# Kernel tuning notes

Measured on AMD Instinct MI355X. Metric: run time of the kernel, lower is better.

## Reference

```python
import jax, jax.numpy as jnp
import numpy as np

B, N_ELEM, N_NODES, E2 = 4096, 2048, 1024, 4096


def setup_inputs() -> dict:
    key = jax.random.key(0)
    k = jax.random.split(key, 7)
    return {
        "EA": jax.random.normal(k[0], (B, N_ELEM), dtype=jnp.float32),
        "e": jax.random.normal(k[1], (B, N_ELEM), dtype=jnp.float32),
        "q": jax.random.normal(k[2], (B, N_NODES, 2), dtype=jnp.float32),
        "r": jax.random.normal(k[3], (B, N_NODES, 2), dtype=jnp.float32),
        "vecs": jax.random.normal(k[4], (E2, 2), dtype=jnp.float32),
        "node_ids": jax.random.randint(k[5], (E2,), 0, N_NODES, dtype=jnp.int32),
        "elem_ids": jax.random.randint(k[6], (E2,), 0, N_ELEM, dtype=jnp.int32),
    }


def reference(EA, e, q, r, vecs, node_ids, elem_ids):
    # axial_forces = EA * e : [B, N_ELEM]
    axial = EA * e
    # gather per incidence entry and scale by the 2-vector: [B, E2, 2]
    contrib = axial[:, elem_ids][..., None] * vecs[None, :, :]
    n_sample, n_nodes = q.shape[0], q.shape[1]
    # scatter-add contributions into per-node residual: [B, N_NODES, 2]
    residual = jnp.zeros((n_sample, n_nodes, 2), dtype=EA.dtype)
    residual = residual.at[:, node_ids, :].add(contrib)
    residual = residual - q - r
    return jnp.mean(jnp.square(residual))
```

## Files before the change

kernel.cpp:

```cpp
#include <hip/hip_runtime.h>

#define B_SAMPLES 4096
#define N_ELEM    2048
#define N_NODES   1024
#define E2        4096
#define BLOCK     512
#define SLOTS     32
#define S         4
#define NPT       (N_NODES / BLOCK)
#define MAIN_BLOCKS (B_SAMPLES / S)

#define WS_CNT_OFF   0
#define WS_ELL_OFF   4096

__global__ __launch_bounds__(256) void neq_zero_kernel(
    float4* __restrict__ ell, int* __restrict__ cnt)
{
    const int i = blockIdx.x * 256 + threadIdx.x;
    ell[i] = make_float4(0.f, 0.f, 0.f, 0.f);
    if (i < N_NODES) cnt[i] = 0;
}

__global__ __launch_bounds__(256) void neq_build_kernel(
    const float* __restrict__ vecs, const int* __restrict__ node_ids,
    const int* __restrict__ elem_ids, int* __restrict__ cnt,
    float4* __restrict__ ell)
{
    const int j = blockIdx.x * 256 + threadIdx.x;
    int nid = node_ids[j];
    int eid = elem_ids[j];
    float2 v = ((const float2*)vecs)[j];
    int slot = atomicAdd(&cnt[nid], 1);
    if (slot < SLOTS) {
        ell[slot * N_NODES + nid] = make_float4(v.x, v.y, __int_as_float(eid), 0.f);
    }
}

__global__ __launch_bounds__(BLOCK, 4) void neq_main_kernel(
    const float* __restrict__ EA, const float* __restrict__ e,
    const float* __restrict__ q,  const float* __restrict__ r,
    const int* __restrict__ cnt, const float4* __restrict__ ell,
    float* __restrict__ out)
{
    __shared__ float4 axial4[N_ELEM];
    __shared__ float red[BLOCK / 64];

    const int b0 = blockIdx.x * S;
    const int t = threadIdx.x;

#pragma unroll
    for (int i = 0; i < N_ELEM / BLOCK; ++i) {
        int eid = t + i * BLOCK;
        float4 p;
        const float* EAp = EA + (size_t)b0 * N_ELEM + eid;
        const float* ep  = e  + (size_t)b0 * N_ELEM + eid;
        p.x = EAp[0 * N_ELEM] * ep[0 * N_ELEM];
        p.y = EAp[1 * N_ELEM] * ep[1 * N_ELEM];
        p.z = EAp[2 * N_ELEM] * ep[2 * N_ELEM];
        p.w = EAp[3 * N_ELEM] * ep[3 * N_ELEM];
        axial4[eid] = p;
    }

    int c0 = min(cnt[t], SLOTS);
    int c1 = min(cnt[t + BLOCK], SLOTS);
    int kmax = max(c0, c1);
    __syncthreads();

    float accx[NPT][S] = {};
    float accy[NPT][S] = {};
    for (int k = 0; k < kmax; ++k) {
        const float4* row = ell + k * N_NODES + t;
#pragma unroll
        for (int i = 0; i < NPT; ++i) {
            int ci = (i == 0) ? c0 : c1;
            if (k < ci) {
                float4 pk = row[i * BLOCK];
                int eid = __float_as_int(pk.z);
                float4 ax = axial4[eid];
                accx[i][0] += ax.x * pk.x;  accy[i][0] += ax.x * pk.y;
                accx[i][1] += ax.y * pk.x;  accy[i][1] += ax.y * pk.y;
                accx[i][2] += ax.z * pk.x;  accy[i][2] += ax.z * pk.y;
                accx[i][3] += ax.w * pk.x;  accy[i][3] += ax.w * pk.y;
            }
        }
    }

    float acc = 0.f;
#pragma unroll
    for (int s = 0; s < S; ++s) {
        const float2* q2 = (const float2*)(q + (size_t)(b0 + s) * N_NODES * 2);
        const float2* r2 = (const float2*)(r + (size_t)(b0 + s) * N_NODES * 2);
#pragma unroll
        for (int i = 0; i < NPT; ++i) {
            int n = t + i * BLOCK;
            float2 qv = q2[n];
            float2 rv = r2[n];
            float x = accx[i][s] - qv.x - rv.x;
            float y = accy[i][s] - qv.y - rv.y;
            acc += x * x + y * y;
        }
    }

#pragma unroll
    for (int off = 32; off > 0; off >>= 1)
        acc += __shfl_down(acc, off, 64);
    if ((t & 63) == 0) red[t >> 6] = acc;
    __syncthreads();
    if (t == 0) {
        float s = 0.f;
#pragma unroll
        for (int w = 0; w < BLOCK / 64; ++w) s += red[w];
        const float inv_n = 1.0f / (float)((size_t)B_SAMPLES * N_NODES * 2);
        atomicAdd(out, s * inv_n);
    }
}

extern "C" void kernel_launch(void* const* d_in, const int* in_sizes, int n_in,
                              void* d_out, int out_size, void* d_ws, size_t ws_size,
                              hipStream_t stream) {
    const float* EA       = (const float*)d_in[0];
    const float* e        = (const float*)d_in[1];
    const float* q        = (const float*)d_in[2];
    const float* r        = (const float*)d_in[3];
    const float* vecs     = (const float*)d_in[4];
    const int*   node_ids = (const int*)d_in[5];
    const int*   elem_ids = (const int*)d_in[6];

    char* ws = (char*)d_ws;
    int*    cnt = (int*)(ws + WS_CNT_OFF);
    float4* ell = (float4*)(ws + WS_ELL_OFF);

    hipMemsetAsync(d_out, 0, sizeof(float), stream);

    neq_zero_kernel<<<(SLOTS * N_NODES) / 256, 256, 0, stream>>>(ell, cnt);
    neq_build_kernel<<<E2 / 256, 256, 0, stream>>>(
        vecs, node_ids, elem_ids, cnt, ell);
    neq_main_kernel<<<MAIN_BLOCKS, BLOCK, 0, stream>>>(
        EA, e, q, r, cnt, ell, (float*)d_out);
}
```

Baseline: 166.6 us.

## Vectorize loads, assign adjacent node pairs per thread, drop ELL zeroing

Each thread now handles two adjacent nodes, so the ELL rows and the q/r residual terms can be read with single float4 loads. Axial forces are stored sample-major in shared memory and EA/e are loaded as float4 instead of strided scalars. The kernel that zeroed the whole ELL buffer is replaced by one that clears only the counters, since slots beyond each count are never read. The cost is four scalar LDS reads per entry instead of one float4, and q values are held in registers across the accumulation loop.

```diff
diff --git a/kernel.cpp b/kernel.cpp
--- a/kernel.cpp
+++ b/kernel.cpp
@@ -7,18 +7,14 @@
 #define BLOCK     512
 #define SLOTS     32
 #define S         4
-#define NPT       (N_NODES / BLOCK)
 #define MAIN_BLOCKS (B_SAMPLES / S)
 
 #define WS_CNT_OFF   0
 #define WS_ELL_OFF   4096
 
-__global__ __launch_bounds__(256) void neq_zero_kernel(
-    float4* __restrict__ ell, int* __restrict__ cnt)
+__global__ __launch_bounds__(N_NODES) void neq_zero_cnt(int* __restrict__ cnt)
 {
-    const int i = blockIdx.x * 256 + threadIdx.x;
-    ell[i] = make_float4(0.f, 0.f, 0.f, 0.f);
-    if (i < N_NODES) cnt[i] = 0;
+    cnt[threadIdx.x] = 0;
 }
 
 __global__ __launch_bounds__(256) void neq_build_kernel(
@@ -36,51 +32,55 @@
     }
 }
 
-__global__ __launch_bounds__(BLOCK, 4) void neq_main_kernel(
+__global__ __launch_bounds__(BLOCK) void neq_main_kernel(
     const float* __restrict__ EA, const float* __restrict__ e,
     const float* __restrict__ q,  const float* __restrict__ r,
     const int* __restrict__ cnt, const float4* __restrict__ ell,
     float* __restrict__ out)
 {
-    __shared__ float4 axial4[N_ELEM];
+    __shared__ float axial[S * N_ELEM];
     __shared__ float red[BLOCK / 64];
 
     const int b0 = blockIdx.x * S;
     const int t = threadIdx.x;
 
 #pragma unroll
-    for (int i = 0; i < N_ELEM / BLOCK; ++i) {
-        int eid = t + i * BLOCK;
-        float4 p;
-        const float* EAp = EA + (size_t)b0 * N_ELEM + eid;
-        const float* ep  = e  + (size_t)b0 * N_ELEM + eid;
-        p.x = EAp[0 * N_ELEM] * ep[0 * N_ELEM];
-        p.y = EAp[1 * N_ELEM] * ep[1 * N_ELEM];
-        p.z = EAp[2 * N_ELEM] * ep[2 * N_ELEM];
-        p.w = EAp[3 * N_ELEM] * ep[3 * N_ELEM];
-        axial4[eid] = p;
+    for (int s = 0; s < S; ++s) {
+        const float4* EA4 = (const float4*)(EA + (size_t)(b0 + s) * N_ELEM);
+        const float4* e4  = (const float4*)(e  + (size_t)(b0 + s) * N_ELEM);
+        float4 a = EA4[t];
+        float4 m = e4[t];
+        ((float4*)(axial + s * N_ELEM))[t] =
+            make_float4(a.x * m.x, a.y * m.y, a.z * m.z, a.w * m.w);
     }
 
-    int c0 = min(cnt[t], SLOTS);
-    int c1 = min(cnt[t + BLOCK], SLOTS);
+    int2 cc = ((const int2*)cnt)[t];
+    int c0 = min(cc.x, SLOTS);
+    int c1 = min(cc.y, SLOTS);
     int kmax = max(c0, c1);
     __syncthreads();
 
-    float accx[NPT][S] = {};
-    float accy[NPT][S] = {};
+    float4 qv[S];
+#pragma unroll
+    for (int s = 0; s < S; ++s)
+        qv[s] = ((const float4*)(q + (size_t)(b0 + s) * N_NODES * 2))[t];
+
+    float accx[2][S] = {};
+    float accy[2][S] = {};
     for (int k = 0; k < kmax; ++k) {
-        const float4* row = ell + k * N_NODES + t;
+        const float4* row = ell + k * N_NODES + 2 * t;
 #pragma unroll
-        for (int i = 0; i < NPT; ++i) {
+        for (int i = 0; i < 2; ++i) {
             int ci = (i == 0) ? c0 : c1;
             if (k < ci) {
-                float4 pk = row[i * BLOCK];
-                int eid = __float_as_int(pk.z);
-                float4 ax = axial4[eid];
-                accx[i][0] += ax.x * pk.x;  accy[i][0] += ax.x * pk.y;
-                accx[i][1] += ax.y * pk.x;  accy[i][1] += ax.y * pk.y;
-                accx[i][2] += ax.z * pk.x;  accy[i][2] += ax.z * pk.y;
-                accx[i][3] += ax.w * pk.x;  accy[i][3] += ax.w * pk.y;
+                float4 w = row[i];
+                int eid = __float_as_int(w.z);
+#pragma unroll
+                for (int s = 0; s < S; ++s) {
+                    float ax = axial[s * N_ELEM + eid];
+                    accx[i][s] += ax * w.x;
+                    accy[i][s] += ax * w.y;
+                }
             }
         }
     }
@@ -88,17 +88,12 @@
     float acc = 0.f;
 #pragma unroll
     for (int s = 0; s < S; ++s) {
-        const float2* q2 = (const float2*)(q + (size_t)(b0 + s) * N_NODES * 2);
-        const float2* r2 = (const float2*)(r + (size_t)(b0 + s) * N_NODES * 2);
-#pragma unroll
-        for (int i = 0; i < NPT; ++i) {
-            int n = t + i * BLOCK;
-            float2 qv = q2[n];
-            float2 rv = r2[n];
-            float x = accx[i][s] - qv.x - rv.x;
-            float y = accy[i][s] - qv.y - rv.y;
-            acc += x * x + y * y;
-        }
+        float4 rv = ((const float4*)(r + (size_t)(b0 + s) * N_NODES * 2))[t];
+        float x0 = accx[0][s] - qv[s].x - rv.x;
+        float y0 = accy[0][s] - qv[s].y - rv.y;
+        float x1 = accx[1][s] - qv[s].z - rv.z;
+        float y1 = accy[1][s] - qv[s].w - rv.w;
+        acc += x0 * x0 + y0 * y0 + x1 * x1 + y1 * y1;
     }
 
 #pragma unroll
@@ -132,7 +127,7 @@
 
     hipMemsetAsync(d_out, 0, sizeof(float), stream);
 
-    neq_zero_kernel<<<(SLOTS * N_NODES) / 256, 256, 0, stream>>>(ell, cnt);
+    neq_zero_cnt<<<1, N_NODES, 0, stream>>>(cnt);
     neq_build_kernel<<<E2 / 256, 256, 0, stream>>>(
         vecs, node_ids, elem_ids, cnt, ell);
     neq_main_kernel<<<MAIN_BLOCKS, BLOCK, 0, stream>>>(
```

Measured after the change: 169.5 us. No clear change (+1.8%).
